# Kernel tuning notes

Hardware: AMD Instinct MI355X
Metric: run time of the kernel (lower is better)

## Reference

```python
import jax, jax.numpy as jnp
import numpy as np
import math

L, D_T, D, NL, NH, FFN, C, B = 24, 1024, 256, 12, 4, 1024, 2, 2048
HD = D // NH


def _layernorm(x, g, b, eps=1e-5):
    m = jnp.mean(x, axis=-1, keepdims=True)
    v = jnp.mean(jnp.square(x - m), axis=-1, keepdims=True)
    return (x - m) * jax.lax.rsqrt(v + eps) * g + b


def _rotate_half(x):
    x1, x2 = jnp.split(x, 2, axis=-1)
    return jnp.concatenate([-x2, x1], axis=-1)


def setup_inputs() -> dict:
    key = jax.random.key(0)
    ks = iter(jax.random.split(key, 64))
    n = lambda shape, s=0.02: jax.random.normal(next(ks), shape, dtype=jnp.float32) * s
    inp = {}
    inp['teacher_cls'] = jax.random.normal(next(ks), (B, L, D_T), dtype=jnp.float32)
    # input LN + projection
    inp['in_ln_g'] = jnp.ones((D_T,), jnp.float32); inp['in_ln_b'] = jnp.zeros((D_T,), jnp.float32)
    inp['proj_w'] = n((D, D_T)); inp['proj_b'] = jnp.zeros((D,), jnp.float32)
    # RoPE caches (buffers)
    inv_freq = 1.0 / (10000.0 ** (np.arange(0, D, 2, dtype=np.float32) / D))
    t = np.arange(L, dtype=np.float32)
    freqs = np.einsum('i,j->ij', t, inv_freq)
    emb = np.concatenate([freqs, freqs], axis=-1)
    inp['cos_cached'] = jnp.asarray(np.cos(emb)[None])  # [1,L,D]
    inp['sin_cached'] = jnp.asarray(np.sin(emb)[None])
    inp['pre_ln_g'] = jnp.ones((D,), jnp.float32); inp['pre_ln_b'] = jnp.zeros((D,), jnp.float32)
    # stacked transformer layer params [NL, ...]
    inp['l_ln1_g'] = jnp.ones((NL, D), jnp.float32); inp['l_ln1_b'] = jnp.zeros((NL, D), jnp.float32)
    inp['l_inw'] = n((NL, 3 * D, D)); inp['l_inb'] = jnp.zeros((NL, 3 * D), jnp.float32)
    inp['l_outw'] = n((NL, D, D)); inp['l_outb'] = jnp.zeros((NL, D), jnp.float32)
    inp['l_ln2_g'] = jnp.ones((NL, D), jnp.float32); inp['l_ln2_b'] = jnp.zeros((NL, D), jnp.float32)
    inp['l_w12'] = n((NL, 2 * FFN, D)); inp['l_b12'] = jnp.zeros((NL, 2 * FFN), jnp.float32)
    inp['l_w3'] = n((NL, D, FFN)); inp['l_b3'] = jnp.zeros((NL, D), jnp.float32)
    inp['post_ln_g'] = jnp.ones((D,), jnp.float32); inp['post_ln_b'] = jnp.zeros((D,), jnp.float32)
    # entropy gate
    inp['eg_w1'] = n((L, D, 8), 0.01); inp['eg_b1'] = jnp.zeros((L, 8), jnp.float32)
    inp['eg_w2'] = n((L, 8, 1), 0.01); inp['eg_b2'] = jnp.zeros((L, 1), jnp.float32)
    # per-position heads (stacked)
    inp['halt_w'] = n((L, D + 1)); inp['halt_b'] = jnp.full((L,), -4.0, jnp.float32)
    inp['cls_w'] = n((L, C, D)); inp['cls_b'] = jnp.zeros((L, C), jnp.float32)
    return inp


def _mha(x, inw, inb, outw, outb, mask):
    Bb, Ll, Dd = x.shape
    qkv = x @ inw.T + inb                              # [B,L,3D]
    q, k, v = jnp.split(qkv, 3, axis=-1)
    def heads(t):
        return t.reshape(Bb, Ll, NH, HD).transpose(0, 2, 1, 3)  # [B,H,L,hd]
    q, k, v = heads(q), heads(k), heads(v)
    scores = jnp.einsum('bhqd,bhkd->bhqk', q, k) / math.sqrt(HD)
    scores = jnp.where(mask, -jnp.inf, scores)
    attn = jax.nn.softmax(scores, axis=-1)
    o = jnp.einsum('bhqk,bhkd->bhqd', attn, v)
    o = o.transpose(0, 2, 1, 3).reshape(Bb, Ll, Dd)
    return o @ outw.T + outb


def reference(teacher_cls, in_ln_g, in_ln_b, proj_w, proj_b, cos_cached, sin_cached,
              pre_ln_g, pre_ln_b, l_ln1_g, l_ln1_b, l_inw, l_inb, l_outw, l_outb,
              l_ln2_g, l_ln2_b, l_w12, l_b12, l_w3, l_b3, post_ln_g, post_ln_b,
              eg_w1, eg_b1, eg_w2, eg_b2, halt_w, halt_b, cls_w, cls_b):
    x = _layernorm(teacher_cls, in_ln_g, in_ln_b)
    x = x @ proj_w.T + proj_b                          # [B,L,D]
    x = x * cos_cached + _rotate_half(x) * sin_cached  # RoPE
    z = _layernorm(x, pre_ln_g, pre_ln_b)
    mask = jnp.triu(jnp.ones((L, L), bool), 1)         # causal
    for i in range(NL):
        xn = _layernorm(z, l_ln1_g[i], l_ln1_b[i])
        z = z + _mha(xn, l_inw[i], l_inb[i], l_outw[i], l_outb[i], mask)
        xn = _layernorm(z, l_ln2_g[i], l_ln2_b[i])
        w12_out = xn @ l_w12[i].T + l_b12[i]           # [B,L,2*FFN]
        x1, x2 = jnp.split(w12_out, 2, axis=-1)
        hidden = jax.nn.silu(x1) * x2
        z = z + hidden @ l_w3[i].T + l_b3[i]
    z = _layernorm(z, post_ln_g, post_ln_b)
    # batched per-position classifier heads
    class_logits = jnp.einsum('bld,lcd->blc', z, cls_w) + cls_b   # [B,L,C]
    log_probs = jax.nn.log_softmax(class_logits, axis=-1)
    probs = jnp.exp(log_probs)
    probs_safe = jnp.clip(probs, 1e-10, 1.0)
    ent = -jnp.sum(probs_safe * jnp.log(probs_safe), axis=-1, keepdims=True)
    ent_norm = jnp.clip(ent / math.log(C), 0.0, 1.0)              # [B,L,1]
    # entropy gate
    h = jnp.tanh(jnp.einsum('bld,ldh->blh', z, eg_w1) + eg_b1)
    gate = jax.nn.sigmoid(jnp.einsum('blh,lho->blo', h, eg_w2) + eg_b2)
    gated = ent_norm * gate                                        # [B,L,1]
    # batched per-position halting heads
    combined = jnp.concatenate([z, gated], axis=-1)                # [B,L,D+1]
    halting_logits = jnp.einsum('bld,ld->bl', combined, halt_w) + halt_b
    return (halting_logits, class_logits, z)
```

## Files before the change

### kernel.cpp

```cpp
#include <hip/hip_runtime.h>
#include <hip/hip_bf16.h>
#include <math.h>

#define L_SEQ 24
#define DT 1024
#define DM 256
#define NLAYER 12
#define NHEAD 4
#define HDIM 64
#define FFND 1024
#define NCLS 2
#define NBATCH 2048
#define NTOK (NBATCH*L_SEQ)

typedef float f32x4 __attribute__((ext_vector_type(4)));
typedef __bf16 bf16x4 __attribute__((ext_vector_type(4)));
typedef __bf16 bf16x8 __attribute__((ext_vector_type(8)));

#define GLDS16(gp, lp) __builtin_amdgcn_global_load_lds((const __attribute__((address_space(1))) void*)(gp), (__attribute__((address_space(3))) void*)(lp), 16, 0, 0)

__device__ inline float wred_sum(float v){
#pragma unroll
  for (int o = 32; o > 0; o >>= 1) v += __shfl_xor(v, o);
  return v;
}
__device__ inline float wred_max(float v){
#pragma unroll
  for (int o = 32; o > 0; o >>= 1) v = fmaxf(v, __shfl_xor(v, o));
  return v;
}

__device__ __forceinline__ void stage8(const __bf16* __restrict__ gtile, int ldk, int k0,
                                       __bf16* lds, int r8, int lane){
  int rloc = (r8 << 3) + (lane >> 3);
  int c = (lane & 7) ^ (rloc & 7);
  GLDS16(gtile + (size_t)rloc*ldk + k0 + c*8, lds + (r8 << 9));
}

__device__ __forceinline__ bf16x8 ldsfrag(const __bf16* tile, int row, int kk, int lane){
  int c = ((kk << 2) + (lane >> 4)) ^ (row & 7);
  return *(const bf16x8*)(tile + (row << 6) + (c << 3));
}

__global__ void cvt_bf16_kernel(const float* __restrict__ in, __bf16* __restrict__ out, int n4){
  int i = blockIdx.x * blockDim.x + threadIdx.x;
  int stride = gridDim.x * blockDim.x;
  for (; i < n4; i += stride){
    float4 v = ((const float4*)in)[i];
    bf16x4 o;
    o[0] = (__bf16)v.x; o[1] = (__bf16)v.y; o[2] = (__bf16)v.z; o[3] = (__bf16)v.w;
    ((bf16x4*)out)[i] = o;
  }
}

__global__ __launch_bounds__(256) void ln1024_kernel(
    const float* __restrict__ in, const float* __restrict__ g, const float* __restrict__ bb,
    __bf16* __restrict__ out){
  int row = blockIdx.x;
  int tid = threadIdx.x, wid = tid >> 6, lane = tid & 63;
  float4 x = ((const float4*)(in + (size_t)row*DT))[tid];
  float s = x.x + x.y + x.z + x.w;
  float q = x.x*x.x + x.y*x.y + x.z*x.z + x.w*x.w;
  s = wred_sum(s); q = wred_sum(q);
  __shared__ float red[8];
  if (lane == 0){ red[wid] = s; red[4+wid] = q; }
  __syncthreads();
  s = red[0]+red[1]+red[2]+red[3];
  q = red[4]+red[5]+red[6]+red[7];
  float mean = s * (1.f/DT);
  float rstd = rsqrtf(q*(1.f/DT) - mean*mean + 1e-5f);
  float4 gv = ((const float4*)g)[tid], bv = ((const float4*)bb)[tid];
  bf16x4 o;
  o[0] = (__bf16)((x.x-mean)*rstd*gv.x + bv.x);
  o[1] = (__bf16)((x.y-mean)*rstd*gv.y + bv.y);
  o[2] = (__bf16)((x.z-mean)*rstd*gv.z + bv.z);
  o[3] = (__bf16)((x.w-mean)*rstd*gv.w + bv.w);
  ((bf16x4*)(out + (size_t)row*DT))[tid] = o;
}

__global__ __launch_bounds__(256) void rope_preln_kernel(
    float* __restrict__ z, const float* __restrict__ cosc, const float* __restrict__ sinc,
    const float* __restrict__ g, const float* __restrict__ bb,
    const float* __restrict__ g1, const float* __restrict__ b1, __bf16* __restrict__ xnb){
  int row = blockIdx.x*4 + (threadIdx.x >> 6);
  int lane = threadIdx.x & 63;
  int l = row % L_SEQ;
  float4 x = ((const float4*)(z + (size_t)row*DM))[lane];
  float4 p;
  p.x = __shfl_xor(x.x, 32); p.y = __shfl_xor(x.y, 32);
  p.z = __shfl_xor(x.z, 32); p.w = __shfl_xor(x.w, 32);
  float sgn = (lane < 32) ? -1.f : 1.f;
  float4 c = ((const float4*)(cosc + l*DM))[lane];
  float4 sn = ((const float4*)(sinc + l*DM))[lane];
  float4 xr;
  xr.x = x.x*c.x + sgn*p.x*sn.x;
  xr.y = x.y*c.y + sgn*p.y*sn.y;
  xr.z = x.z*c.z + sgn*p.z*sn.z;
  xr.w = x.w*c.w + sgn*p.w*sn.w;
  float s = wred_sum(xr.x + xr.y + xr.z + xr.w);
  float q = wred_sum(xr.x*xr.x + xr.y*xr.y + xr.z*xr.z + xr.w*xr.w);
  float mean = s * (1.f/DM);
  float rstd = rsqrtf(q*(1.f/DM) - mean*mean + 1e-5f);
  float4 gv = ((const float4*)g)[lane], bv = ((const float4*)bb)[lane];
  float4 y;
  y.x = (xr.x-mean)*rstd*gv.x + bv.x;
  y.y = (xr.y-mean)*rstd*gv.y + bv.y;
  y.z = (xr.z-mean)*rstd*gv.z + bv.z;
  y.w = (xr.w-mean)*rstd*gv.w + bv.w;
  ((float4*)(z + (size_t)row*DM))[lane] = y;
  float s2 = wred_sum(y.x + y.y + y.z + y.w);
  float q2 = wred_sum(y.x*y.x + y.y*y.y + y.z*y.z + y.w*y.w);
  float mean2 = s2 * (1.f/DM);
  float rstd2 = rsqrtf(q2*(1.f/DM) - mean2*mean2 + 1e-5f);
  float4 g1v = ((const float4*)g1)[lane], b1v = ((const float4*)b1)[lane];
  bf16x4 o;
  o[0] = (__bf16)((y.x-mean2)*rstd2*g1v.x + b1v.x);
  o[1] = (__bf16)((y.y-mean2)*rstd2*g1v.y + b1v.y);
  o[2] = (__bf16)((y.z-mean2)*rstd2*g1v.z + b1v.z);
  o[3] = (__bf16)((y.w-mean2)*rstd2*g1v.w + b1v.w);
  ((bf16x4*)(xnb + (size_t)row*DM))[lane] = o;
}

template<int MODE>
__global__ __launch_bounds__(256) void gemm128_kernel(
    const __bf16* __restrict__ A, const __bf16* __restrict__ W,
    const float* __restrict__ bias,
    float* __restrict__ Cf, __bf16* __restrict__ Cb,
    int N, int K, int nt){
  __shared__ __align__(16) __bf16 As[128*64];
  __shared__ __align__(16) __bf16 Bs[128*64];
  int bm = blockIdx.x / nt, bn = blockIdx.x % nt;
  int tid = threadIdx.x, wid = tid >> 6, lane = tid & 63;
  int wr = wid >> 1, wc = wid & 1;
  f32x4 acc[4][4] = {};
  const __bf16* ga = A + (size_t)bm*128*K;
  const __bf16* gb = W + (size_t)bn*128*K;
  for (int k0 = 0; k0 < K; k0 += 64){
#pragma unroll
    for (int j = 0; j < 4; j++) stage8(ga, K, k0, As, wid*4 + j, lane);
#pragma unroll
    for (int j = 0; j < 4; j++) stage8(gb, K, k0, Bs, wid*4 + j, lane);
    __syncthreads();
#pragma unroll
    for (int kk = 0; kk < 2; kk++){
      bf16x8 af[4], bfr[4];
#pragma unroll
      for (int mi = 0; mi < 4; mi++) af[mi]  = ldsfrag(As, wr*64 + mi*16 + (lane&15), kk, lane);
#pragma unroll
      for (int ni = 0; ni < 4; ni++) bfr[ni] = ldsfrag(Bs, wc*64 + ni*16 + (lane&15), kk, lane);
#pragma unroll
      for (int mi = 0; mi < 4; mi++)
#pragma unroll
        for (int ni = 0; ni < 4; ni++)
          acc[mi][ni] = __builtin_amdgcn_mfma_f32_16x16x32_bf16(af[mi], bfr[ni], acc[mi][ni], 0, 0, 0);
    }
    __syncthreads();
  }
  int colbase = bn*128 + wc*64 + (lane & 15);
  int rowbase = bm*128 + wr*64 + ((lane >> 4) << 2);
#pragma unroll
  for (int mi = 0; mi < 4; mi++){
#pragma unroll
    for (int ni = 0; ni < 4; ni++){
      int col = colbase + ni*16;
      float bv = bias[col];
      int m0 = rowbase + mi*16;
#pragma unroll
      for (int r = 0; r < 4; r++){
        float v = acc[mi][ni][r] + bv;
        size_t idx = (size_t)(m0 + r)*N + col;
        if (MODE == 0) Cf[idx] = v;
        else Cb[idx] = (__bf16)v;
      }
    }
  }
}

__global__ __launch_bounds__(256) void gemm_glu_kernel(
    const __bf16* __restrict__ A, const __bf16* __restrict__ W12,
    const float* __restrict__ bias, __bf16* __restrict__ H){
  __shared__ __align__(16) __bf16 As[128*64];
  __shared__ __align__(16) __bf16 B1s[128*64];
  __shared__ __align__(16) __bf16 B2s[128*64];
  const int K = 256;
  int bm = blockIdx.x >> 3, bn = blockIdx.x & 7;
  int tid = threadIdx.x, wid = tid >> 6, lane = tid & 63;
  int wr = wid >> 1, wc = wid & 1;
  f32x4 acc1[4][4] = {}, acc2[4][4] = {};
  const __bf16* ga  = A   + (size_t)bm*128*K;
  const __bf16* gb1 = W12 + (size_t)bn*128*K;
  const __bf16* gb2 = gb1 + (size_t)1024*K;
  for (int k0 = 0; k0 < K; k0 += 64){
#pragma unroll
    for (int j = 0; j < 4; j++) stage8(ga,  K, k0, As,  wid*4 + j, lane);
#pragma unroll
    for (int j = 0; j < 4; j++) stage8(gb1, K, k0, B1s, wid*4 + j, lane);
#pragma unroll
    for (int j = 0; j < 4; j++) stage8(gb2, K, k0, B2s, wid*4 + j, lane);
    __syncthreads();
#pragma unroll
    for (int kk = 0; kk < 2; kk++){
      bf16x8 af[4], b1f[4], b2f[4];
#pragma unroll
      for (int mi = 0; mi < 4; mi++) af[mi]  = ldsfrag(As,  wr*64 + mi*16 + (lane&15), kk, lane);
#pragma unroll
      for (int ni = 0; ni < 4; ni++){
        b1f[ni] = ldsfrag(B1s, wc*64 + ni*16 + (lane&15), kk, lane);
        b2f[ni] = ldsfrag(B2s, wc*64 + ni*16 + (lane&15), kk, lane);
      }
#pragma unroll
      for (int mi = 0; mi < 4; mi++)
#pragma unroll
        for (int ni = 0; ni < 4; ni++){
          acc1[mi][ni] = __builtin_amdgcn_mfma_f32_16x16x32_bf16(af[mi], b1f[ni], acc1[mi][ni], 0, 0, 0);
          acc2[mi][ni] = __builtin_amdgcn_mfma_f32_16x16x32_bf16(af[mi], b2f[ni], acc2[mi][ni], 0, 0, 0);
        }
    }
    __syncthreads();
  }
  int colbase = bn*128 + wc*64 + (lane & 15);
  int rowbase = bm*128 + wr*64 + ((lane >> 4) << 2);
#pragma unroll
  for (int mi = 0; mi < 4; mi++)
#pragma unroll
    for (int ni = 0; ni < 4; ni++){
      int col = colbase + ni*16;
      float b1 = bias[col], b2 = bias[1024 + col];
      int m0 = rowbase + mi*16;
#pragma unroll
      for (int r = 0; r < 4; r++){
        float v1 = acc1[mi][ni][r] + b1;
        float v2 = acc2[mi][ni][r] + b2;
        float sig = 1.f/(1.f + __expf(-v1));
        H[(size_t)(m0 + r)*FFND + col] = (__bf16)(v1*sig*v2);
      }
    }
}

__global__ __launch_bounds__(256) void gemm_ln_kernel(
    const __bf16* __restrict__ A, const __bf16* __restrict__ W,
    const float* __restrict__ bias, float* __restrict__ z,
    const float* __restrict__ lng, const float* __restrict__ lnb,
    __bf16* __restrict__ outb, float* __restrict__ outf, int K){
  __shared__ __align__(16) __bf16 As[64*64];
  __shared__ __align__(16) __bf16 Bs[256*64];
  __shared__ float redS[64][4], redQ[64][4];
  int bm = blockIdx.x;
  int tid = threadIdx.x, wid = tid >> 6, lane = tid & 63;
  const __bf16* ga = A + (size_t)bm*64*K;
  f32x4 acc[4][4] = {};
  for (int k0 = 0; k0 < K; k0 += 64){
#pragma unroll
    for (int j = 0; j < 2; j++) stage8(ga, K, k0, As, wid*2 + j, lane);
#pragma unroll
    for (int j = 0; j < 8; j++) stage8(W,  K, k0, Bs, wid*8 + j, lane);
    __syncthreads();
#pragma unroll
    for (int kk = 0; kk < 2; kk++){
      bf16x8 af[4], bfr[4];
#pragma unroll
      for (int mi = 0; mi < 4; mi++) af[mi]  = ldsfrag(As, mi*16 + (lane&15), kk, lane);
#pragma unroll
      for (int ni = 0; ni < 4; ni++) bfr[ni] = ldsfrag(Bs, wid*64 + ni*16 + (lane&15), kk, lane);
#pragma unroll
      for (int mi = 0; mi < 4; mi++)
#pragma unroll
        for (int ni = 0; ni < 4; ni++)
          acc[mi][ni] = __builtin_amdgcn_mfma_f32_16x16x32_bf16(af[mi], bfr[ni], acc[mi][ni], 0, 0, 0);
    }
    __syncthreads();
  }
  int g = lane >> 4, li = lane & 15;
  float sA[4][4] = {}, qA[4][4] = {};
#pragma unroll
  for (int mi = 0; mi < 4; mi++)
#pragma unroll
    for (int r = 0; r < 4; r++){
      int rl = mi*16 + g*4 + r;
      size_t rowg = (size_t)(bm*64 + rl)*DM;
#pragma unroll
      for (int ni = 0; ni < 4; ni++){
        int col = wid*64 + ni*16 + li;
        float v = acc[mi][ni][r] + bias[col] + z[rowg + col];
        acc[mi][ni][r] = v;
        z[rowg + col] = v;
        sA[mi][r] += v; qA[mi][r] += v*v;
      }
    }
#pragma unroll
  for (int mi = 0; mi < 4; mi++)
#pragma unroll
    for (int r = 0; r < 4; r++){
      float s = sA[mi][r], q = qA[mi][r];
#pragma unroll
      for (int off = 1; off < 16; off <<= 1){ s += __shfl_xor(s, off); q += __shfl_xor(q, off); }
      if (li == 0){ redS[mi*16 + g*4 + r][wid] = s; redQ[mi*16 + g*4 + r][wid] = q; }
    }
  __syncthreads();
#pragma unroll
  for (int mi = 0; mi < 4; mi++)
#pragma unroll
    for (int r = 0; r < 4; r++){
      int rl = mi*16 + g*4 + r;
      float s = redS[rl][0] + redS[rl][1] + redS[rl][2] + redS[rl][3];
      float q = redQ[rl][0] + redQ[rl][1] + redQ[rl][2] + redQ[rl][3];
      float mean = s * (1.f/DM);
      float rstd = rsqrtf(q*(1.f/DM) - mean*mean + 1e-5f);
      size_t rowg = (size_t)(bm*64 + rl)*DM;
#pragma unroll
      for (int ni = 0; ni < 4; ni++){
        int col = wid*64 + ni*16 + li;
        float xn = (acc[mi][ni][r] - mean)*rstd*lng[col] + lnb[col];
        if (outb) outb[rowg + col] = (__bf16)xn;
        else      outf[rowg + col] = xn;
      }
    }
}

__global__ __launch_bounds__(256) void attn_kernel(const __bf16* __restrict__ qkv, __bf16* __restrict__ ob){
  int b = blockIdx.x;
  int h = threadIdx.x >> 6, lane = threadIdx.x & 63;
  __shared__ __align__(16) __bf16 Qs[NHEAD][L_SEQ][HDIM];
  __shared__ __align__(16) __bf16 Ks[NHEAD][L_SEQ][HDIM];
  __shared__ float Ps[NHEAD][L_SEQ][L_SEQ];
  const __bf16* base = qkv + (size_t)b*L_SEQ*768;
  float V[L_SEQ];
#pragma unroll
  for (int t = 0; t < L_SEQ; t++){
    int sw = lane ^ ((t & 7) << 3);
    Qs[h][t][sw] = base[t*768 + h*64 + lane];
    Ks[h][t][sw] = base[t*768 + 256 + h*64 + lane];
    V[t] = (float)base[t*768 + 512 + h*64 + lane];
  }
  __syncthreads();
  for (int p = lane; p < L_SEQ*L_SEQ; p += 64){
    int q = p / L_SEQ, k = p - q*L_SEQ;
    if (k <= q){
      int qx = (q & 7) << 3, kx = (k & 7) << 3;
      const __bf16* qr = Qs[h][q];
      const __bf16* kr = Ks[h][k];
      float s = 0.f;
#pragma unroll
      for (int d = 0; d < 64; d += 4){
        bf16x4 qa = *(const bf16x4*)(qr + (d ^ qx));
        bf16x4 ka = *(const bf16x4*)(kr + (d ^ kx));
        s += (float)qa[0]*(float)ka[0] + (float)qa[1]*(float)ka[1]
           + (float)qa[2]*(float)ka[2] + (float)qa[3]*(float)ka[3];
      }
      Ps[h][q][k] = s * 0.125f;
    }
  }
  __syncthreads();
  for (int q = 0; q < L_SEQ; q++){
    float v = (lane <= q) ? Ps[h][q][lane] : -1e30f;
    float mx = wred_max(v);
    float e = (lane <= q) ? __expf(v - mx) : 0.f;
    float sm = wred_sum(e);
    if (lane < L_SEQ) Ps[h][q][lane] = e / sm;
  }
  __syncthreads();
  for (int q = 0; q < L_SEQ; q++){
    float o = 0.f;
    for (int k = 0; k <= q; k++) o += Ps[h][q][k] * V[k];
    ob[((size_t)b*L_SEQ + q)*DM + h*64 + lane] = (__bf16)o;
  }
}

__global__ __launch_bounds__(256) void heads_kernel(
    const float* __restrict__ z,
    const float* __restrict__ cls_w, const float* __restrict__ cls_b,
    const float* __restrict__ eg_w1, const float* __restrict__ eg_b1,
    const float* __restrict__ eg_w2, const float* __restrict__ eg_b2,
    const float* __restrict__ halt_w, const float* __restrict__ halt_b,
    float* __restrict__ halt_out, float* __restrict__ cls_out){
  int m = blockIdx.x*4 + (threadIdx.x >> 6);
  int lane = threadIdx.x & 63;
  int l = m % L_SEQ;
  float4 zv = ((const float4*)(z + (size_t)m*DM))[lane];
  float4 w0 = ((const float4*)(cls_w + ((size_t)l*2 + 0)*DM))[lane];
  float4 w1 = ((const float4*)(cls_w + ((size_t)l*2 + 1)*DM))[lane];
  float c0 = wred_sum(zv.x*w0.x + zv.y*w0.y + zv.z*w0.z + zv.w*w0.w) + cls_b[l*2 + 0];
  float c1 = wred_sum(zv.x*w1.x + zv.y*w1.y + zv.z*w1.z + zv.w*w1.w) + cls_b[l*2 + 1];
  float mx = fmaxf(c0, c1);
  float e0 = __expf(c0 - mx), e1 = __expf(c1 - mx);
  float inv = 1.f/(e0 + e1);
  float p0 = fminf(fmaxf(e0*inv, 1e-10f), 1.f);
  float p1 = fminf(fmaxf(e1*inv, 1e-10f), 1.f);
  float ent = -(p0*__logf(p0) + p1*__logf(p1));
  float entn = fminf(fmaxf(ent * 1.44269504f, 0.f), 1.f);
  const float4* wg = (const float4*)(eg_w1 + ((size_t)l*DM + 4*lane)*8);
  float hacc[8] = {};
#pragma unroll
  for (int dd = 0; dd < 4; dd++){
    float zd = (dd==0) ? zv.x : (dd==1) ? zv.y : (dd==2) ? zv.z : zv.w;
    float4 a = wg[dd*2], b = wg[dd*2 + 1];
    hacc[0] += zd*a.x; hacc[1] += zd*a.y; hacc[2] += zd*a.z; hacc[3] += zd*a.w;
    hacc[4] += zd*b.x; hacc[5] += zd*b.y; hacc[6] += zd*b.z; hacc[7] += zd*b.w;
  }
  float gin = 0.f;
#pragma unroll
  for (int j = 0; j < 8; j++){
    float hj = wred_sum(hacc[j]);
    hj = tanhf(hj + eg_b1[l*8 + j]);
    gin += hj * eg_w2[l*8 + j];
  }
  gin += eg_b2[l];
  float gate = 1.f/(1.f + __expf(-gin));
  float gated = entn * gate;
  const float* hw = halt_w + (size_t)l*257;
  float hp = zv.x*hw[4*lane] + zv.y*hw[4*lane+1] + zv.z*hw[4*lane+2] + zv.w*hw[4*lane+3];
  float hl = wred_sum(hp) + gated*hw[256] + halt_b[l];
  if (lane == 0) halt_out[m] = hl;
  if (lane < 2) cls_out[(size_t)m*2 + lane] = lane ? c1 : c0;
}

extern "C" void kernel_launch(void* const* d_in, const int* in_sizes, int n_in,
                              void* d_out, int out_size, void* d_ws, size_t ws_size,
                              hipStream_t stream){
  const float* teacher = (const float*)d_in[0];
  const float* in_ln_g = (const float*)d_in[1];
  const float* in_ln_b = (const float*)d_in[2];
  const float* proj_w  = (const float*)d_in[3];
  const float* proj_b  = (const float*)d_in[4];
  const float* cosc    = (const float*)d_in[5];
  const float* sinc    = (const float*)d_in[6];
  const float* pre_g   = (const float*)d_in[7];
  const float* pre_b   = (const float*)d_in[8];
  const float* l_ln1_g = (const float*)d_in[9];
  const float* l_ln1_b = (const float*)d_in[10];
  const float* l_inw   = (const float*)d_in[11];
  const float* l_inb   = (const float*)d_in[12];
  const float* l_outw  = (const float*)d_in[13];
  const float* l_outb  = (const float*)d_in[14];
  const float* l_ln2_g = (const float*)d_in[15];
  const float* l_ln2_b = (const float*)d_in[16];
  const float* l_w12   = (const float*)d_in[17];
  const float* l_b12   = (const float*)d_in[18];
  const float* l_w3    = (const float*)d_in[19];
  const float* l_b3    = (const float*)d_in[20];
  const float* post_g  = (const float*)d_in[21];
  const float* post_b  = (const float*)d_in[22];
  const float* eg_w1   = (const float*)d_in[23];
  const float* eg_b1   = (const float*)d_in[24];
  const float* eg_w2   = (const float*)d_in[25];
  const float* eg_b2   = (const float*)d_in[26];
  const float* halt_w  = (const float*)d_in[27];
  const float* halt_b  = (const float*)d_in[28];
  const float* cls_w   = (const float*)d_in[29];
  const float* cls_b   = (const float*)d_in[30];

  float* out = (float*)d_out;
  float* halt_out = out;
  float* cls_out  = out + NTOK;
  float* z_out    = out + NTOK + (size_t)NTOK*NCLS;

  char* ws = (char*)d_ws;
  size_t off = 0;
  auto alloc = [&](size_t bytes){ void* p = ws + off; off += (bytes + 255) & ~(size_t)255; return p; };
  float*  zbuf = (float*) alloc((size_t)NTOK*DM*4);
  __bf16* xnb  = (__bf16*)alloc((size_t)NTOK*DM*2);
  __bf16* qkvb = (__bf16*)alloc((size_t)NTOK*768*2);
  __bf16* obuf = (__bf16*)alloc((size_t)NTOK*DM*2);
  __bf16* bigb = (__bf16*)alloc((size_t)NTOK*1024*2);
  __bf16* w_proj = (__bf16*)alloc((size_t)262144*2);
  __bf16* w_in   = (__bf16*)alloc((size_t)2359296*2);
  __bf16* w_out  = (__bf16*)alloc((size_t)786432*2);
  __bf16* w_12   = (__bf16*)alloc((size_t)6291456*2);
  __bf16* w_3    = (__bf16*)alloc((size_t)3145728*2);

  cvt_bf16_kernel<<<256, 256, 0, stream>>>(proj_w, w_proj, 262144/4);
  cvt_bf16_kernel<<<1024, 256, 0, stream>>>(l_inw, w_in, 2359296/4);
  cvt_bf16_kernel<<<512, 256, 0, stream>>>(l_outw, w_out, 786432/4);
  cvt_bf16_kernel<<<2048, 256, 0, stream>>>(l_w12, w_12, 6291456/4);
  cvt_bf16_kernel<<<1024, 256, 0, stream>>>(l_w3, w_3, 3145728/4);

  ln1024_kernel<<<NTOK, 256, 0, stream>>>(teacher, in_ln_g, in_ln_b, bigb);
  gemm128_kernel<0><<<384*2, 256, 0, stream>>>(bigb, w_proj, proj_b, zbuf, nullptr, 256, 1024, 2);
  rope_preln_kernel<<<NTOK/4, 256, 0, stream>>>(zbuf, cosc, sinc, pre_g, pre_b, l_ln1_g, l_ln1_b, xnb);

  for (int i = 0; i < NLAYER; i++){
    gemm128_kernel<1><<<384*6, 256, 0, stream>>>(xnb, w_in + (size_t)i*768*256, l_inb + i*768, nullptr, qkvb, 768, 256, 6);
    attn_kernel<<<NBATCH, 256, 0, stream>>>(qkvb, obuf);
    gemm_ln_kernel<<<NTOK/64, 256, 0, stream>>>(obuf, w_out + (size_t)i*256*256, l_outb + i*256,
                                                zbuf, l_ln2_g + i*256, l_ln2_b + i*256, xnb, nullptr, 256);
    gemm_glu_kernel<<<384*8, 256, 0, stream>>>(xnb, w_12 + (size_t)i*2048*256, l_b12 + i*2048, bigb);
    bool last = (i == NLAYER-1);
    gemm_ln_kernel<<<NTOK/64, 256, 0, stream>>>(bigb, w_3 + (size_t)i*256*1024, l_b3 + i*256,
                                                zbuf,
                                                last ? post_g : l_ln1_g + (i+1)*256,
                                                last ? post_b : l_ln1_b + (i+1)*256,
                                                last ? nullptr : xnb,
                                                last ? z_out : nullptr, 1024);
  }

  heads_kernel<<<NTOK/4, 256, 0, stream>>>(z_out, cls_w, cls_b, eg_w1, eg_b1, eg_w2, eg_b2,
                                           halt_w, halt_b, halt_out, cls_out);
}
```

Baseline: 4.437 ms.

## Load GEMM MFMA fragments directly from global memory, dropping LDS staging

All three GEMM kernel families stop staging A and B tiles into LDS through global_load_lds and the barriers around it. Each wave now loads its bf16x8 MFMA fragments straight from global memory, and K becomes a template parameter so the loop fully specialises. This removes the LDS round trip and the two __syncthreads per K step. In exchange, operands shared between waves are fetched separately by each wave through L1/L2 rather than once into LDS, and the row-strided 16-byte loads may coalesce worse.

```diff
diff --git a/kernel.cpp b/kernel.cpp
--- a/kernel.cpp
+++ b/kernel.cpp
@@ -17,8 +17,6 @@
 typedef __bf16 bf16x4 __attribute__((ext_vector_type(4)));
 typedef __bf16 bf16x8 __attribute__((ext_vector_type(8)));
 
-#define GLDS16(gp, lp) __builtin_amdgcn_global_load_lds((const __attribute__((address_space(1))) void*)(gp), (__attribute__((address_space(3))) void*)(lp), 16, 0, 0)
-
 __device__ inline float wred_sum(float v){
 #pragma unroll
   for (int o = 32; o > 0; o >>= 1) v += __shfl_xor(v, o);
@@ -28,18 +26,6 @@
 #pragma unroll
   for (int o = 32; o > 0; o >>= 1) v = fmaxf(v, __shfl_xor(v, o));
   return v;
-}
-
-__device__ __forceinline__ void stage8(const __bf16* __restrict__ gtile, int ldk, int k0,
-                                       __bf16* lds, int r8, int lane){
-  int rloc = (r8 << 3) + (lane >> 3);
-  int c = (lane & 7) ^ (rloc & 7);
-  GLDS16(gtile + (size_t)rloc*ldk + k0 + c*8, lds + (r8 << 9));
-}
-
-__device__ __forceinline__ bf16x8 ldsfrag(const __bf16* tile, int row, int kk, int lane){
-  int c = ((kk << 2) + (lane >> 4)) ^ (row & 7);
-  return *(const bf16x8*)(tile + (row << 6) + (c << 3));
 }
 
 __global__ void cvt_bf16_kernel(const float* __restrict__ in, __bf16* __restrict__ out, int n4){
@@ -121,40 +107,30 @@
   ((bf16x4*)(xnb + (size_t)row*DM))[lane] = o;
 }
 
-template<int MODE>
+template<int MODE, int K>
 __global__ __launch_bounds__(256) void gemm128_kernel(
     const __bf16* __restrict__ A, const __bf16* __restrict__ W,
     const float* __restrict__ bias,
     float* __restrict__ Cf, __bf16* __restrict__ Cb,
-    int N, int K, int nt){
-  __shared__ __align__(16) __bf16 As[128*64];
-  __shared__ __align__(16) __bf16 Bs[128*64];
+    int N, int nt){
   int bm = blockIdx.x / nt, bn = blockIdx.x % nt;
-  int tid = threadIdx.x, wid = tid >> 6, lane = tid & 63;
+  int wid = threadIdx.x >> 6, lane = threadIdx.x & 63;
   int wr = wid >> 1, wc = wid & 1;
   f32x4 acc[4][4] = {};
-  const __bf16* ga = A + (size_t)bm*128*K;
-  const __bf16* gb = W + (size_t)bn*128*K;
-  for (int k0 = 0; k0 < K; k0 += 64){
-#pragma unroll
-    for (int j = 0; j < 4; j++) stage8(ga, K, k0, As, wid*4 + j, lane);
-#pragma unroll
-    for (int j = 0; j < 4; j++) stage8(gb, K, k0, Bs, wid*4 + j, lane);
-    __syncthreads();
-#pragma unroll
-    for (int kk = 0; kk < 2; kk++){
-      bf16x8 af[4], bfr[4];
-#pragma unroll
-      for (int mi = 0; mi < 4; mi++) af[mi]  = ldsfrag(As, wr*64 + mi*16 + (lane&15), kk, lane);
-#pragma unroll
-      for (int ni = 0; ni < 4; ni++) bfr[ni] = ldsfrag(Bs, wc*64 + ni*16 + (lane&15), kk, lane);
-#pragma unroll
-      for (int mi = 0; mi < 4; mi++)
-#pragma unroll
-        for (int ni = 0; ni < 4; ni++)
-          acc[mi][ni] = __builtin_amdgcn_mfma_f32_16x16x32_bf16(af[mi], bfr[ni], acc[mi][ni], 0, 0, 0);
-    }
-    __syncthreads();
+  const __bf16* pa = A + (size_t)(bm*128 + wr*64 + (lane&15))*K + ((lane>>4)<<3);
+  const __bf16* pb = W + (size_t)(bn*128 + wc*64 + (lane&15))*K + ((lane>>4)<<3);
+#pragma unroll 2
+  for (int k = 0; k < K; k += 32){
+    bf16x8 af[4], bfr[4];
+#pragma unroll
+    for (int mi = 0; mi < 4; mi++) af[mi]  = *(const bf16x8*)(pa + mi*16*K + k);
+#pragma unroll
+    for (int ni = 0; ni < 4; ni++) bfr[ni] = *(const bf16x8*)(pb + ni*16*K + k);
+#pragma unroll
+    for (int mi = 0; mi < 4; mi++)
+#pragma unroll
+      for (int ni = 0; ni < 4; ni++)
+        acc[mi][ni] = __builtin_amdgcn_mfma_f32_16x16x32_bf16(af[mi], bfr[ni], acc[mi][ni], 0, 0, 0);
   }
   int colbase = bn*128 + wc*64 + (lane & 15);
   int rowbase = bm*128 + wr*64 + ((lane >> 4) << 2);
@@ -179,44 +155,30 @@
 __global__ __launch_bounds__(256) void gemm_glu_kernel(
     const __bf16* __restrict__ A, const __bf16* __restrict__ W12,
     const float* __restrict__ bias, __bf16* __restrict__ H){
-  __shared__ __align__(16) __bf16 As[128*64];
-  __shared__ __align__(16) __bf16 B1s[128*64];
-  __shared__ __align__(16) __bf16 B2s[128*64];
   const int K = 256;
   int bm = blockIdx.x >> 3, bn = blockIdx.x & 7;
-  int tid = threadIdx.x, wid = tid >> 6, lane = tid & 63;
+  int wid = threadIdx.x >> 6, lane = threadIdx.x & 63;
   int wr = wid >> 1, wc = wid & 1;
   f32x4 acc1[4][4] = {}, acc2[4][4] = {};
-  const __bf16* ga  = A   + (size_t)bm*128*K;
-  const __bf16* gb1 = W12 + (size_t)bn*128*K;
-  const __bf16* gb2 = gb1 + (size_t)1024*K;
-  for (int k0 = 0; k0 < K; k0 += 64){
-#pragma unroll
-    for (int j = 0; j < 4; j++) stage8(ga,  K, k0, As,  wid*4 + j, lane);
-#pragma unroll
-    for (int j = 0; j < 4; j++) stage8(gb1, K, k0, B1s, wid*4 + j, lane);
-#pragma unroll
-    for (int j = 0; j < 4; j++) stage8(gb2, K, k0, B2s, wid*4 + j, lane);
-    __syncthreads();
-#pragma unroll
-    for (int kk = 0; kk < 2; kk++){
-      bf16x8 af[4], b1f[4], b2f[4];
-#pragma unroll
-      for (int mi = 0; mi < 4; mi++) af[mi]  = ldsfrag(As,  wr*64 + mi*16 + (lane&15), kk, lane);
+  const __bf16* pa  = A   + (size_t)(bm*128 + wr*64 + (lane&15))*K + ((lane>>4)<<3);
+  const __bf16* pb1 = W12 + (size_t)(bn*128 + wc*64 + (lane&15))*K + ((lane>>4)<<3);
+  const __bf16* pb2 = pb1 + (size_t)1024*K;
+#pragma unroll 2
+  for (int k = 0; k < K; k += 32){
+    bf16x8 af[4], b1f[4], b2f[4];
+#pragma unroll
+    for (int mi = 0; mi < 4; mi++) af[mi]  = *(const bf16x8*)(pa  + mi*16*K + k);
+#pragma unroll
+    for (int ni = 0; ni < 4; ni++) b1f[ni] = *(const bf16x8*)(pb1 + ni*16*K + k);
+#pragma unroll
+    for (int ni = 0; ni < 4; ni++) b2f[ni] = *(const bf16x8*)(pb2 + ni*16*K + k);
+#pragma unroll
+    for (int mi = 0; mi < 4; mi++)
 #pragma unroll
       for (int ni = 0; ni < 4; ni++){
-        b1f[ni] = ldsfrag(B1s, wc*64 + ni*16 + (lane&15), kk, lane);
-        b2f[ni] = ldsfrag(B2s, wc*64 + ni*16 + (lane&15), kk, lane);
-      }
-#pragma unroll
-      for (int mi = 0; mi < 4; mi++)
-#pragma unroll
-        for (int ni = 0; ni < 4; ni++){
-          acc1[mi][ni] = __builtin_amdgcn_mfma_f32_16x16x32_bf16(af[mi], b1f[ni], acc1[mi][ni], 0, 0, 0);
-          acc2[mi][ni] = __builtin_amdgcn_mfma_f32_16x16x32_bf16(af[mi], b2f[ni], acc2[mi][ni], 0, 0, 0);
-        }
-    }
-    __syncthreads();
+        acc1[mi][ni] = __builtin_amdgcn_mfma_f32_16x16x32_bf16(af[mi], b1f[ni], acc1[mi][ni], 0, 0, 0);
+        acc2[mi][ni] = __builtin_amdgcn_mfma_f32_16x16x32_bf16(af[mi], b2f[ni], acc2[mi][ni], 0, 0, 0);
+      }
   }
   int colbase = bn*128 + wc*64 + (lane & 15);
   int rowbase = bm*128 + wr*64 + ((lane >> 4) << 2);
@@ -237,38 +199,30 @@
     }
 }
 
+template<int K>
 __global__ __launch_bounds__(256) void gemm_ln_kernel(
     const __bf16* __restrict__ A, const __bf16* __restrict__ W,
     const float* __restrict__ bias, float* __restrict__ z,
     const float* __restrict__ lng, const float* __restrict__ lnb,
-    __bf16* __restrict__ outb, float* __restrict__ outf, int K){
-  __shared__ __align__(16) __bf16 As[64*64];
-  __shared__ __align__(16) __bf16 Bs[256*64];
+    __bf16* __restrict__ outb, float* __restrict__ outf){
   __shared__ float redS[64][4], redQ[64][4];
   int bm = blockIdx.x;
-  int tid = threadIdx.x, wid = tid >> 6, lane = tid & 63;
-  const __bf16* ga = A + (size_t)bm*64*K;
+  int wid = threadIdx.x >> 6, lane = threadIdx.x & 63;
   f32x4 acc[4][4] = {};
-  for (int k0 = 0; k0 < K; k0 += 64){
-#pragma unroll
-    for (int j = 0; j < 2; j++) stage8(ga, K, k0, As, wid*2 + j, lane);
-#pragma unroll
-    for (int j = 0; j < 8; j++) stage8(W,  K, k0, Bs, wid*8 + j, lane);
-    __syncthreads();
-#pragma unroll
-    for (int kk = 0; kk < 2; kk++){
-      bf16x8 af[4], bfr[4];
-#pragma unroll
-      for (int mi = 0; mi < 4; mi++) af[mi]  = ldsfrag(As, mi*16 + (lane&15), kk, lane);
-#pragma unroll
-      for (int ni = 0; ni < 4; ni++) bfr[ni] = ldsfrag(Bs, wid*64 + ni*16 + (lane&15), kk, lane);
-#pragma unroll
-      for (int mi = 0; mi < 4; mi++)
-#pragma unroll
-        for (int ni = 0; ni < 4; ni++)
-          acc[mi][ni] = __builtin_amdgcn_mfma_f32_16x16x32_bf16(af[mi], bfr[ni], acc[mi][ni], 0, 0, 0);
-    }
-    __syncthreads();
+  const __bf16* pa = A + (size_t)(bm*64 + (lane&15))*K + ((lane>>4)<<3);
+  const __bf16* pb = W + (size_t)(wid*64 + (lane&15))*K + ((lane>>4)<<3);
+#pragma unroll 2
+  for (int k = 0; k < K; k += 32){
+    bf16x8 af[4], bfr[4];
+#pragma unroll
+    for (int mi = 0; mi < 4; mi++) af[mi]  = *(const bf16x8*)(pa + mi*16*K + k);
+#pragma unroll
+    for (int ni = 0; ni < 4; ni++) bfr[ni] = *(const bf16x8*)(pb + ni*16*K + k);
+#pragma unroll
+    for (int mi = 0; mi < 4; mi++)
+#pragma unroll
+      for (int ni = 0; ni < 4; ni++)
+        acc[mi][ni] = __builtin_amdgcn_mfma_f32_16x16x32_bf16(af[mi], bfr[ni], acc[mi][ni], 0, 0, 0);
   }
   int g = lane >> 4, li = lane & 15;
   float sA[4][4] = {}, qA[4][4] = {};
@@ -475,22 +429,22 @@
   cvt_bf16_kernel<<<1024, 256, 0, stream>>>(l_w3, w_3, 3145728/4);
 
   ln1024_kernel<<<NTOK, 256, 0, stream>>>(teacher, in_ln_g, in_ln_b, bigb);
-  gemm128_kernel<0><<<384*2, 256, 0, stream>>>(bigb, w_proj, proj_b, zbuf, nullptr, 256, 1024, 2);
+  gemm128_kernel<0, 1024><<<384*2, 256, 0, stream>>>(bigb, w_proj, proj_b, zbuf, nullptr, 256, 2);
   rope_preln_kernel<<<NTOK/4, 256, 0, stream>>>(zbuf, cosc, sinc, pre_g, pre_b, l_ln1_g, l_ln1_b, xnb);
 
   for (int i = 0; i < NLAYER; i++){
-    gemm128_kernel<1><<<384*6, 256, 0, stream>>>(xnb, w_in + (size_t)i*768*256, l_inb + i*768, nullptr, qkvb, 768, 256, 6);
+    gemm128_kernel<1, 256><<<384*6, 256, 0, stream>>>(xnb, w_in + (size_t)i*768*256, l_inb + i*768, nullptr, qkvb, 768, 6);
     attn_kernel<<<NBATCH, 256, 0, stream>>>(qkvb, obuf);
-    gemm_ln_kernel<<<NTOK/64, 256, 0, stream>>>(obuf, w_out + (size_t)i*256*256, l_outb + i*256,
-                                                zbuf, l_ln2_g + i*256, l_ln2_b + i*256, xnb, nullptr, 256);
+    gemm_ln_kernel<256><<<NTOK/64, 256, 0, stream>>>(obuf, w_out + (size_t)i*256*256, l_outb + i*256,
+                                                     zbuf, l_ln2_g + i*256, l_ln2_b + i*256, xnb, nullptr);
     gemm_glu_kernel<<<384*8, 256, 0, stream>>>(xnb, w_12 + (size_t)i*2048*256, l_b12 + i*2048, bigb);
     bool last = (i == NLAYER-1);
-    gemm_ln_kernel<<<NTOK/64, 256, 0, stream>>>(bigb, w_3 + (size_t)i*256*1024, l_b3 + i*256,
-                                                zbuf,
-                                                last ? post_g : l_ln1_g + (i+1)*256,
-                                                last ? post_b : l_ln1_b + (i+1)*256,
-                                                last ? nullptr : xnb,
-                                                last ? z_out : nullptr, 1024);
+    gemm_ln_kernel<1024><<<NTOK/64, 256, 0, stream>>>(bigb, w_3 + (size_t)i*256*1024, l_b3 + i*256,
+                                                      zbuf,
+                                                      last ? post_g : l_ln1_g + (i+1)*256,
+                                                      last ? post_b : l_ln1_b + (i+1)*256,
+                                                      last ? nullptr : xnb,
+                                                      last ? z_out : nullptr);
   }
 
   heads_kernel<<<NTOK/4, 256, 0, stream>>>(z_out, cls_w, cls_b, eg_w1, eg_b1, eg_w2, eg_b2,
```

After: 6.760 ms. +52.4%, slower.

## Enlarge GEMM tiles to 256x128 with 512 threads and transpose MFMA for vector stores

Applied to the files above, without the earlier changes.

The projection, QKV and GLU GEMMs move to 256-row tiles with 8 waves per block, halving the grid and sharing each weight tile across more rows. MFMA operands are swapped (weights as A, activations as B), so each lane holds four consecutive output columns. The epilogues can then use vectorized bias loads and f32x4/bf16x4 stores, and the LN reduction needs fewer shuffles. K is made a template parameter so the loop fully unrolls. In exchange, register and LDS pressure per block rise, and launch_bounds(512,2) may cause spills.

```diff
diff --git a/kernel.cpp b/kernel.cpp
--- a/kernel.cpp
+++ b/kernel.cpp
@@ -30,11 +30,11 @@
   return v;
 }
 
-__device__ __forceinline__ void stage8(const __bf16* __restrict__ gtile, int ldk, int k0,
-                                       __bf16* lds, int r8, int lane){
-  int rloc = (r8 << 3) + (lane >> 3);
-  int c = (lane & 7) ^ (rloc & 7);
-  GLDS16(gtile + (size_t)rloc*ldk + k0 + c*8, lds + (r8 << 9));
+__device__ __forceinline__ void stageG(const __bf16* __restrict__ gtile, int ldk, int k0,
+                                       __bf16* lds_wavebase, int lane, int rowbase){
+  int row = rowbase + (lane >> 3);
+  int c = (lane & 7) ^ (row & 7);
+  GLDS16(gtile + (size_t)row*ldk + k0 + c*8, lds_wavebase);
 }
 
 __device__ __forceinline__ bf16x8 ldsfrag(const __bf16* tile, int row, int kk, int lane){
@@ -121,200 +121,210 @@
   ((bf16x4*)(xnb + (size_t)row*DM))[lane] = o;
 }
 
-template<int MODE>
-__global__ __launch_bounds__(256) void gemm128_kernel(
+template<int MODE, int K>
+__global__ __launch_bounds__(512, 2) void gemm512_kernel(
     const __bf16* __restrict__ A, const __bf16* __restrict__ W,
     const float* __restrict__ bias,
     float* __restrict__ Cf, __bf16* __restrict__ Cb,
-    int N, int K, int nt){
-  __shared__ __align__(16) __bf16 As[128*64];
+    int N, int nt){
+  __shared__ __align__(16) __bf16 As[256*64];
   __shared__ __align__(16) __bf16 Bs[128*64];
   int bm = blockIdx.x / nt, bn = blockIdx.x % nt;
   int tid = threadIdx.x, wid = tid >> 6, lane = tid & 63;
   int wr = wid >> 1, wc = wid & 1;
+  int li = lane & 15, g4 = (lane >> 4) << 2;
   f32x4 acc[4][4] = {};
-  const __bf16* ga = A + (size_t)bm*128*K;
+  const __bf16* ga = A + (size_t)bm*256*K;
   const __bf16* gb = W + (size_t)bn*128*K;
   for (int k0 = 0; k0 < K; k0 += 64){
 #pragma unroll
-    for (int j = 0; j < 4; j++) stage8(ga, K, k0, As, wid*4 + j, lane);
-#pragma unroll
-    for (int j = 0; j < 4; j++) stage8(gb, K, k0, Bs, wid*4 + j, lane);
+    for (int j = 0; j < 4; j++){ int rb = j*64 + wid*8; stageG(ga, K, k0, As + (rb<<6), lane, rb); }
+#pragma unroll
+    for (int j = 0; j < 2; j++){ int rb = j*64 + wid*8; stageG(gb, K, k0, Bs + (rb<<6), lane, rb); }
     __syncthreads();
 #pragma unroll
     for (int kk = 0; kk < 2; kk++){
-      bf16x8 af[4], bfr[4];
-#pragma unroll
-      for (int mi = 0; mi < 4; mi++) af[mi]  = ldsfrag(As, wr*64 + mi*16 + (lane&15), kk, lane);
-#pragma unroll
-      for (int ni = 0; ni < 4; ni++) bfr[ni] = ldsfrag(Bs, wc*64 + ni*16 + (lane&15), kk, lane);
-#pragma unroll
-      for (int mi = 0; mi < 4; mi++)
-#pragma unroll
-        for (int ni = 0; ni < 4; ni++)
-          acc[mi][ni] = __builtin_amdgcn_mfma_f32_16x16x32_bf16(af[mi], bfr[ni], acc[mi][ni], 0, 0, 0);
+      bf16x8 xf[4], wf[4];
+#pragma unroll
+      for (int mi = 0; mi < 4; mi++) xf[mi] = ldsfrag(As, wr*64 + mi*16 + li, kk, lane);
+#pragma unroll
+      for (int ni = 0; ni < 4; ni++) wf[ni] = ldsfrag(Bs, wc*64 + ni*16 + li, kk, lane);
+#pragma unroll
+      for (int ni = 0; ni < 4; ni++)
+#pragma unroll
+        for (int mi = 0; mi < 4; mi++)
+          acc[ni][mi] = __builtin_amdgcn_mfma_f32_16x16x32_bf16(wf[ni], xf[mi], acc[ni][mi], 0, 0, 0);
     }
     __syncthreads();
   }
-  int colbase = bn*128 + wc*64 + (lane & 15);
-  int rowbase = bm*128 + wr*64 + ((lane >> 4) << 2);
 #pragma unroll
   for (int mi = 0; mi < 4; mi++){
+    int m = bm*256 + wr*64 + mi*16 + li;
 #pragma unroll
     for (int ni = 0; ni < 4; ni++){
-      int col = colbase + ni*16;
-      float bv = bias[col];
-      int m0 = rowbase + mi*16;
-#pragma unroll
-      for (int r = 0; r < 4; r++){
-        float v = acc[mi][ni][r] + bv;
-        size_t idx = (size_t)(m0 + r)*N + col;
-        if (MODE == 0) Cf[idx] = v;
-        else Cb[idx] = (__bf16)v;
+      int n = bn*128 + wc*64 + ni*16 + g4;
+      f32x4 bv = *(const f32x4*)(bias + n);
+      f32x4 o = acc[ni][mi] + bv;
+      if (MODE == 0){
+        *(f32x4*)(Cf + (size_t)m*N + n) = o;
+      } else {
+        bf16x4 ob;
+        ob[0] = (__bf16)o[0]; ob[1] = (__bf16)o[1]; ob[2] = (__bf16)o[2]; ob[3] = (__bf16)o[3];
+        *(bf16x4*)(Cb + (size_t)m*N + n) = ob;
       }
     }
   }
 }
 
-__global__ __launch_bounds__(256) void gemm_glu_kernel(
+__global__ __launch_bounds__(512, 2) void gemm_glu_kernel(
     const __bf16* __restrict__ A, const __bf16* __restrict__ W12,
     const float* __restrict__ bias, __bf16* __restrict__ H){
-  __shared__ __align__(16) __bf16 As[128*64];
+  __shared__ __align__(16) __bf16 As[256*64];
   __shared__ __align__(16) __bf16 B1s[128*64];
   __shared__ __align__(16) __bf16 B2s[128*64];
   const int K = 256;
   int bm = blockIdx.x >> 3, bn = blockIdx.x & 7;
   int tid = threadIdx.x, wid = tid >> 6, lane = tid & 63;
   int wr = wid >> 1, wc = wid & 1;
+  int li = lane & 15, g4 = (lane >> 4) << 2;
   f32x4 acc1[4][4] = {}, acc2[4][4] = {};
-  const __bf16* ga  = A   + (size_t)bm*128*K;
+  const __bf16* ga  = A   + (size_t)bm*256*K;
   const __bf16* gb1 = W12 + (size_t)bn*128*K;
   const __bf16* gb2 = gb1 + (size_t)1024*K;
   for (int k0 = 0; k0 < K; k0 += 64){
 #pragma unroll
-    for (int j = 0; j < 4; j++) stage8(ga,  K, k0, As,  wid*4 + j, lane);
-#pragma unroll
-    for (int j = 0; j < 4; j++) stage8(gb1, K, k0, B1s, wid*4 + j, lane);
-#pragma unroll
-    for (int j = 0; j < 4; j++) stage8(gb2, K, k0, B2s, wid*4 + j, lane);
+    for (int j = 0; j < 4; j++){ int rb = j*64 + wid*8; stageG(ga,  K, k0, As  + (rb<<6), lane, rb); }
+#pragma unroll
+    for (int j = 0; j < 2; j++){ int rb = j*64 + wid*8; stageG(gb1, K, k0, B1s + (rb<<6), lane, rb); }
+#pragma unroll
+    for (int j = 0; j < 2; j++){ int rb = j*64 + wid*8; stageG(gb2, K, k0, B2s + (rb<<6), lane, rb); }
     __syncthreads();
 #pragma unroll
     for (int kk = 0; kk < 2; kk++){
-      bf16x8 af[4], b1f[4], b2f[4];
-#pragma unroll
-      for (int mi = 0; mi < 4; mi++) af[mi]  = ldsfrag(As,  wr*64 + mi*16 + (lane&15), kk, lane);
+      bf16x8 xf[4], w1f[4], w2f[4];
+#pragma unroll
+      for (int mi = 0; mi < 4; mi++) xf[mi] = ldsfrag(As, wr*64 + mi*16 + li, kk, lane);
 #pragma unroll
       for (int ni = 0; ni < 4; ni++){
-        b1f[ni] = ldsfrag(B1s, wc*64 + ni*16 + (lane&15), kk, lane);
-        b2f[ni] = ldsfrag(B2s, wc*64 + ni*16 + (lane&15), kk, lane);
+        w1f[ni] = ldsfrag(B1s, wc*64 + ni*16 + li, kk, lane);
+        w2f[ni] = ldsfrag(B2s, wc*64 + ni*16 + li, kk, lane);
       }
 #pragma unroll
-      for (int mi = 0; mi < 4; mi++)
-#pragma unroll
-        for (int ni = 0; ni < 4; ni++){
-          acc1[mi][ni] = __builtin_amdgcn_mfma_f32_16x16x32_bf16(af[mi], b1f[ni], acc1[mi][ni], 0, 0, 0);
-          acc2[mi][ni] = __builtin_amdgcn_mfma_f32_16x16x32_bf16(af[mi], b2f[ni], acc2[mi][ni], 0, 0, 0);
+      for (int ni = 0; ni < 4; ni++)
+#pragma unroll
+        for (int mi = 0; mi < 4; mi++){
+          acc1[ni][mi] = __builtin_amdgcn_mfma_f32_16x16x32_bf16(w1f[ni], xf[mi], acc1[ni][mi], 0, 0, 0);
+          acc2[ni][mi] = __builtin_amdgcn_mfma_f32_16x16x32_bf16(w2f[ni], xf[mi], acc2[ni][mi], 0, 0, 0);
         }
     }
     __syncthreads();
   }
-  int colbase = bn*128 + wc*64 + (lane & 15);
-  int rowbase = bm*128 + wr*64 + ((lane >> 4) << 2);
-#pragma unroll
-  for (int mi = 0; mi < 4; mi++)
+#pragma unroll
+  for (int mi = 0; mi < 4; mi++){
+    int m = bm*256 + wr*64 + mi*16 + li;
 #pragma unroll
     for (int ni = 0; ni < 4; ni++){
-      int col = colbase + ni*16;
-      float b1 = bias[col], b2 = bias[1024 + col];
-      int m0 = rowbase + mi*16;
+      int n = bn*128 + wc*64 + ni*16 + g4;
+      f32x4 b1v = *(const f32x4*)(bias + n);
+      f32x4 b2v = *(const f32x4*)(bias + 1024 + n);
+      bf16x4 ob;
 #pragma unroll
       for (int r = 0; r < 4; r++){
-        float v1 = acc1[mi][ni][r] + b1;
-        float v2 = acc2[mi][ni][r] + b2;
+        float v1 = acc1[ni][mi][r] + b1v[r];
+        float v2 = acc2[ni][mi][r] + b2v[r];
         float sig = 1.f/(1.f + __expf(-v1));
-        H[(size_t)(m0 + r)*FFND + col] = (__bf16)(v1*sig*v2);
+        ob[r] = (__bf16)(v1*sig*v2);
       }
-    }
-}
-
+      *(bf16x4*)(H + (size_t)m*FFND + n) = ob;
+    }
+  }
+}
+
+template<int K>
 __global__ __launch_bounds__(256) void gemm_ln_kernel(
     const __bf16* __restrict__ A, const __bf16* __restrict__ W,
     const float* __restrict__ bias, float* __restrict__ z,
     const float* __restrict__ lng, const float* __restrict__ lnb,
-    __bf16* __restrict__ outb, float* __restrict__ outf, int K){
+    __bf16* __restrict__ outb, float* __restrict__ outf){
   __shared__ __align__(16) __bf16 As[64*64];
   __shared__ __align__(16) __bf16 Bs[256*64];
   __shared__ float redS[64][4], redQ[64][4];
   int bm = blockIdx.x;
-  int tid = threadIdx.x, wid = tid >> 6, lane = tid & 63;
+  int wid = threadIdx.x >> 6, lane = threadIdx.x & 63;
+  int li = lane & 15, g4 = (lane >> 4) << 2;
+  f32x4 acc[4][4] = {};
   const __bf16* ga = A + (size_t)bm*64*K;
-  f32x4 acc[4][4] = {};
   for (int k0 = 0; k0 < K; k0 += 64){
 #pragma unroll
-    for (int j = 0; j < 2; j++) stage8(ga, K, k0, As, wid*2 + j, lane);
-#pragma unroll
-    for (int j = 0; j < 8; j++) stage8(W,  K, k0, Bs, wid*8 + j, lane);
+    for (int j = 0; j < 2; j++){ int rb = j*32 + wid*8; stageG(ga, K, k0, As + (rb<<6), lane, rb); }
+#pragma unroll
+    for (int j = 0; j < 8; j++){ int rb = j*32 + wid*8; stageG(W,  K, k0, Bs + (rb<<6), lane, rb); }
     __syncthreads();
 #pragma unroll
     for (int kk = 0; kk < 2; kk++){
-      bf16x8 af[4], bfr[4];
-#pragma unroll
-      for (int mi = 0; mi < 4; mi++) af[mi]  = ldsfrag(As, mi*16 + (lane&15), kk, lane);
-#pragma unroll
-      for (int ni = 0; ni < 4; ni++) bfr[ni] = ldsfrag(Bs, wid*64 + ni*16 + (lane&15), kk, lane);
-#pragma unroll
-      for (int mi = 0; mi < 4; mi++)
-#pragma unroll
-        for (int ni = 0; ni < 4; ni++)
-          acc[mi][ni] = __builtin_amdgcn_mfma_f32_16x16x32_bf16(af[mi], bfr[ni], acc[mi][ni], 0, 0, 0);
+      bf16x8 xf[4], wf[4];
+#pragma unroll
+      for (int mi = 0; mi < 4; mi++) xf[mi] = ldsfrag(As, mi*16 + li, kk, lane);
+#pragma unroll
+      for (int ni = 0; ni < 4; ni++) wf[ni] = ldsfrag(Bs, wid*64 + ni*16 + li, kk, lane);
+#pragma unroll
+      for (int ni = 0; ni < 4; ni++)
+#pragma unroll
+        for (int mi = 0; mi < 4; mi++)
+          acc[ni][mi] = __builtin_amdgcn_mfma_f32_16x16x32_bf16(wf[ni], xf[mi], acc[ni][mi], 0, 0, 0);
     }
     __syncthreads();
   }
-  int g = lane >> 4, li = lane & 15;
-  float sA[4][4] = {}, qA[4][4] = {};
-#pragma unroll
-  for (int mi = 0; mi < 4; mi++)
-#pragma unroll
-    for (int r = 0; r < 4; r++){
-      int rl = mi*16 + g*4 + r;
-      size_t rowg = (size_t)(bm*64 + rl)*DM;
-#pragma unroll
-      for (int ni = 0; ni < 4; ni++){
-        int col = wid*64 + ni*16 + li;
-        float v = acc[mi][ni][r] + bias[col] + z[rowg + col];
-        acc[mi][ni][r] = v;
-        z[rowg + col] = v;
-        sA[mi][r] += v; qA[mi][r] += v*v;
+  float sA[4] = {}, qA[4] = {};
+#pragma unroll
+  for (int mi = 0; mi < 4; mi++){
+    int m = bm*64 + mi*16 + li;
+#pragma unroll
+    for (int ni = 0; ni < 4; ni++){
+      int n = wid*64 + ni*16 + g4;
+      f32x4 zv = *(const f32x4*)(z + (size_t)m*DM + n);
+      f32x4 bv = *(const f32x4*)(bias + n);
+      f32x4 v = acc[ni][mi] + bv + zv;
+      acc[ni][mi] = v;
+      *(f32x4*)(z + (size_t)m*DM + n) = v;
+#pragma unroll
+      for (int r = 0; r < 4; r++){ sA[mi] += v[r]; qA[mi] += v[r]*v[r]; }
+    }
+  }
+#pragma unroll
+  for (int mi = 0; mi < 4; mi++){
+    float s = sA[mi], q = qA[mi];
+    s += __shfl_xor(s, 16); q += __shfl_xor(q, 16);
+    s += __shfl_xor(s, 32); q += __shfl_xor(q, 32);
+    if ((lane >> 4) == 0){ redS[mi*16 + li][wid] = s; redQ[mi*16 + li][wid] = q; }
+  }
+  __syncthreads();
+#pragma unroll
+  for (int mi = 0; mi < 4; mi++){
+    int ml = mi*16 + li;
+    float s = redS[ml][0] + redS[ml][1] + redS[ml][2] + redS[ml][3];
+    float q = redQ[ml][0] + redQ[ml][1] + redQ[ml][2] + redQ[ml][3];
+    float mean = s * (1.f/DM);
+    float rstd = rsqrtf(q*(1.f/DM) - mean*mean + 1e-5f);
+    int m = bm*64 + ml;
+#pragma unroll
+    for (int ni = 0; ni < 4; ni++){
+      int n = wid*64 + ni*16 + g4;
+      f32x4 gv = *(const f32x4*)(lng + n);
+      f32x4 bv = *(const f32x4*)(lnb + n);
+      if (outb){
+        bf16x4 o;
+#pragma unroll
+        for (int r = 0; r < 4; r++) o[r] = (__bf16)((acc[ni][mi][r] - mean)*rstd*gv[r] + bv[r]);
+        *(bf16x4*)(outb + (size_t)m*DM + n) = o;
+      } else {
+        f32x4 o;
+#pragma unroll
+        for (int r = 0; r < 4; r++) o[r] = (acc[ni][mi][r] - mean)*rstd*gv[r] + bv[r];
+        *(f32x4*)(outf + (size_t)m*DM + n) = o;
       }
     }
-#pragma unroll
-  for (int mi = 0; mi < 4; mi++)
-#pragma unroll
-    for (int r = 0; r < 4; r++){
-      float s = sA[mi][r], q = qA[mi][r];
-#pragma unroll
-      for (int off = 1; off < 16; off <<= 1){ s += __shfl_xor(s, off); q += __shfl_xor(q, off); }
-      if (li == 0){ redS[mi*16 + g*4 + r][wid] = s; redQ[mi*16 + g*4 + r][wid] = q; }
-    }
-  __syncthreads();
-#pragma unroll
-  for (int mi = 0; mi < 4; mi++)
-#pragma unroll
-    for (int r = 0; r < 4; r++){
-      int rl = mi*16 + g*4 + r;
-      float s = redS[rl][0] + redS[rl][1] + redS[rl][2] + redS[rl][3];
-      float q = redQ[rl][0] + redQ[rl][1] + redQ[rl][2] + redQ[rl][3];
-      float mean = s * (1.f/DM);
-      float rstd = rsqrtf(q*(1.f/DM) - mean*mean + 1e-5f);
-      size_t rowg = (size_t)(bm*64 + rl)*DM;
-#pragma unroll
-      for (int ni = 0; ni < 4; ni++){
-        int col = wid*64 + ni*16 + li;
-        float xn = (acc[mi][ni][r] - mean)*rstd*lng[col] + lnb[col];
-        if (outb) outb[rowg + col] = (__bf16)xn;
-        else      outf[rowg + col] = xn;
-      }
-    }
+  }
 }
 
 __global__ __launch_bounds__(256) void attn_kernel(const __bf16* __restrict__ qkv, __bf16* __restrict__ ob){
@@ -475,22 +485,22 @@
   cvt_bf16_kernel<<<1024, 256, 0, stream>>>(l_w3, w_3, 3145728/4);
 
   ln1024_kernel<<<NTOK, 256, 0, stream>>>(teacher, in_ln_g, in_ln_b, bigb);
-  gemm128_kernel<0><<<384*2, 256, 0, stream>>>(bigb, w_proj, proj_b, zbuf, nullptr, 256, 1024, 2);
+  gemm512_kernel<0, 1024><<<192*2, 512, 0, stream>>>(bigb, w_proj, proj_b, zbuf, nullptr, 256, 2);
   rope_preln_kernel<<<NTOK/4, 256, 0, stream>>>(zbuf, cosc, sinc, pre_g, pre_b, l_ln1_g, l_ln1_b, xnb);
 
   for (int i = 0; i < NLAYER; i++){
-    gemm128_kernel<1><<<384*6, 256, 0, stream>>>(xnb, w_in + (size_t)i*768*256, l_inb + i*768, nullptr, qkvb, 768, 256, 6);
+    gemm512_kernel<1, 256><<<192*6, 512, 0, stream>>>(xnb, w_in + (size_t)i*768*256, l_inb + i*768, nullptr, qkvb, 768, 6);
     attn_kernel<<<NBATCH, 256, 0, stream>>>(qkvb, obuf);
-    gemm_ln_kernel<<<NTOK/64, 256, 0, stream>>>(obuf, w_out + (size_t)i*256*256, l_outb + i*256,
-                                                zbuf, l_ln2_g + i*256, l_ln2_b + i*256, xnb, nullptr, 256);
-    gemm_glu_kernel<<<384*8, 256, 0, stream>>>(xnb, w_12 + (size_t)i*2048*256, l_b12 + i*2048, bigb);
+    gemm_ln_kernel<256><<<NTOK/64, 256, 0, stream>>>(obuf, w_out + (size_t)i*256*256, l_outb + i*256,
+                                                     zbuf, l_ln2_g + i*256, l_ln2_b + i*256, xnb, nullptr);
+    gemm_glu_kernel<<<192*8, 512, 0, stream>>>(xnb, w_12 + (size_t)i*2048*256, l_b12 + i*2048, bigb);
     bool last = (i == NLAYER-1);
-    gemm_ln_kernel<<<NTOK/64, 256, 0, stream>>>(bigb, w_3 + (size_t)i*256*1024, l_b3 + i*256,
-                                                zbuf,
-                                                last ? post_g : l_ln1_g + (i+1)*256,
-                                                last ? post_b : l_ln1_b + (i+1)*256,
-                                                last ? nullptr : xnb,
-                                                last ? z_out : nullptr, 1024);
+    gemm_ln_kernel<1024><<<NTOK/64, 256, 0, stream>>>(bigb, w_3 + (size_t)i*256*1024, l_b3 + i*256,
+                                                      zbuf,
+                                                      last ? post_g : l_ln1_g + (i+1)*256,
+                                                      last ? post_b : l_ln1_b + (i+1)*256,
+                                                      last ? nullptr : xnb,
+                                                      last ? z_out : nullptr);
   }
 
   heads_kernel<<<NTOK/4, 256, 0, stream>>>(z_out, cls_w, cls_b, eg_w1, eg_b1, eg_w2, eg_b2,
```

Measured after the change: 4.095 ms. 7.7% less time.
